# Kernel optimization log

Hardware: AMD Instinct MI355X
Metric: run time of the kernel (lower is better)

Reference implementation:

```python
import jax, jax.numpy as jnp
import numpy as np

B, H, W, C_IN, F = 4, 64, 64, 128, 256


def setup_inputs() -> dict:
    key = jax.random.key(0)
    ks = jax.random.split(key, 6)
    return {
        "inputs": jax.random.normal(ks[0], (B, H, W, C_IN), dtype=jnp.float32),
        "W_proj": jax.random.normal(ks[1], (C_IN, F), dtype=jnp.float32) * 0.02,
        "b_proj": jnp.zeros((F,), dtype=jnp.float32),
        "W_q": jax.random.normal(ks[2], (F, F), dtype=jnp.float32) * 0.02,
        "b_q": jnp.zeros((F,), dtype=jnp.float32),
        "W_k": jax.random.normal(ks[3], (F, F), dtype=jnp.float32) * 0.02,
        "b_k": jnp.zeros((F,), dtype=jnp.float32),
        "W_v": jax.random.normal(ks[4], (F, F), dtype=jnp.float32) * 0.02,
        "b_v": jnp.zeros((F,), dtype=jnp.float32),
        "gamma": jax.random.uniform(ks[5], (1,), dtype=jnp.float32),
    }


def reference(inputs, W_proj, b_proj, W_q, b_q, W_k, b_k, W_v, b_v, gamma):
    # 1x1 conv projection (C_in -> filters) since input channels != filters
    x = jnp.einsum("bhwc,cf->bhwf", inputs, W_proj) + b_proj  # [B,H,W,F]
    q = jnp.einsum("bhwf,fg->bhwg", x, W_q) + b_q
    k = jnp.einsum("bhwf,fg->bhwg", x, W_k) + b_k
    v = jnp.einsum("bhwf,fg->bhwg", x, W_v) + b_v
    b, h, w, f = x.shape
    n = h * w
    qr = q.reshape(b, n, f)
    kr = k.reshape(b, n, f)
    vr = v.reshape(b, n, f)
    attn = jax.nn.softmax(jnp.einsum("bnf,bmf->bnm", qr, kr), axis=-1)  # [B,N,N]
    context = jnp.einsum("bnm,bmf->bnf", attn, vr).reshape(b, h, w, f)
    return gamma * context + x
```

## Files before the change

kernel.cpp:

```cpp
#include <hip/hip_runtime.h>
#include <hip/hip_bf16.h>
#include <stdint.h>

typedef __attribute__((ext_vector_type(8))) short short8;
typedef __attribute__((ext_vector_type(4))) float floatx4;
typedef __attribute__((ext_vector_type(16))) float floatx16;
typedef __attribute__((ext_vector_type(2))) long longx2;

#define DEVI __device__ __forceinline__
#define MFMA16(a, b, c) __builtin_amdgcn_mfma_f32_16x16x32_bf16((a), (b), (c), 0, 0, 0)
#define MFMA32(a, b, c) __builtin_amdgcn_mfma_f32_32x32x16_fp8_fp8((a), (b), (c), 0, 0, 0)

typedef __attribute__((address_space(3))) unsigned int lds_u32;
typedef __attribute__((address_space(1))) const unsigned int glb_u32;
#define GLOAD_LDS16(g, l) __builtin_amdgcn_global_load_lds((glb_u32*)(g), (lds_u32*)(l), 16, 0, 0)

DEVI unsigned short f2bf(float x) {
    union { float f; unsigned int u; } v; v.f = x;
    unsigned int r = v.u + 0x7FFFu + ((v.u >> 16) & 1u);
    return (unsigned short)(r >> 16);
}
DEVI float bf2f(unsigned short h) {
    union { unsigned int u; float f; } v; v.u = ((unsigned int)h) << 16;
    return v.f;
}
DEVI unsigned char f2fp8(float x) {
    int c = __builtin_amdgcn_cvt_pk_fp8_f32(x, x, 0, false);
    return (unsigned char)(c & 0xFF);
}

__global__ __launch_bounds__(256) void prep_weights(
    const float* __restrict__ Wp, const float* __restrict__ Wq,
    const float* __restrict__ Wk, const float* __restrict__ Wv,
    unsigned short* __restrict__ Tp, unsigned short* __restrict__ Tq,
    unsigned short* __restrict__ Tk, unsigned short* __restrict__ Tv)
{
    __shared__ unsigned short Tl[64][72];
    const int bb = blockIdx.x;
    const float* W; unsigned short* T; int K; int tt;
    if (bb < 8)       { W = Wp; T = Tp; K = 128; tt = bb;      }
    else if (bb < 24) { W = Wq; T = Tq; K = 256; tt = bb - 8;  }
    else if (bb < 40) { W = Wk; T = Tk; K = 256; tt = bb - 24; }
    else              { W = Wv; T = Tv; K = 256; tt = bb - 40; }
    const int r0 = (tt >> 2) * 64;
    const int c0 = (tt & 3) * 64;
    const int tid = threadIdx.x;

    #pragma unroll
    for (int i = 0; i < 4; ++i) {
        int u = tid + i * 256;
        int r = u >> 4, c4 = u & 15;
        float4 v = *(const float4*)&W[(size_t)(r0 + r) * 256 + c0 + c4 * 4];
        Tl[c4 * 4 + 0][r] = f2bf(v.x);
        Tl[c4 * 4 + 1][r] = f2bf(v.y);
        Tl[c4 * 4 + 2][r] = f2bf(v.z);
        Tl[c4 * 4 + 3][r] = f2bf(v.w);
    }
    __syncthreads();
    #pragma unroll
    for (int i = 0; i < 2; ++i) {
        int u = tid + i * 256;
        int orow = u >> 3, g = u & 7;
        *(short8*)&T[(size_t)(c0 + orow) * K + r0 + g * 8] = *(const short8*)&Tl[orow][g * 8];
    }
}


__global__ __launch_bounds__(256) void gemm_bias(
    const float* __restrict__ A,
    const unsigned short* __restrict__ Wt,
    const float* __restrict__ bias,
    unsigned short* __restrict__ Cb,
    int N)
{
    __shared__ __align__(16) unsigned short As[64][136];
    __shared__ __align__(16) unsigned short Bs[64][136];
    const int tid  = threadIdx.x;
    const int w    = tid >> 6;
    const int lane = tid & 63;
    const int quad = lane >> 4;
    const int l15  = lane & 15;
    const int m0 = blockIdx.x * 64;
    const int n0 = blockIdx.y * 64;

    floatx4 acc[4];
    #pragma unroll
    for (int t = 0; t < 4; ++t) acc[t] = (floatx4)0.0f;

    #pragma unroll
    for (int it = 0; it < 8; ++it) {
        int idx = tid + it * 256;
        int r = idx >> 5, c4 = idx & 31;
        float4 v = *(const float4*)&A[(size_t)(m0 + r) * 128 + c4 * 4];
        ushort4 o;
        o.x = f2bf(v.x); o.y = f2bf(v.y); o.z = f2bf(v.z); o.w = f2bf(v.w);
        *(ushort4*)&As[r][c4 * 4] = o;
    }
    #pragma unroll
    for (int it = 0; it < 4; ++it) {
        int idx = tid + it * 256;
        int r = idx >> 4, g = idx & 15;
        *(short8*)&Bs[r][g * 8] = *(const short8*)&Wt[(size_t)(n0 + r) * 128 + g * 8];
    }
    __syncthreads();
    #pragma unroll
    for (int s = 0; s < 4; ++s) {
        short8 a = *(const short8*)&As[w * 16 + l15][s * 32 + quad * 8];
        #pragma unroll
        for (int t = 0; t < 4; ++t) {
            short8 bfr = *(const short8*)&Bs[t * 16 + l15][s * 32 + quad * 8];
            acc[t] = MFMA16(a, bfr, acc[t]);
        }
    }

    __syncthreads();
    unsigned short* T = &As[0][0];
    #pragma unroll
    for (int t = 0; t < 4; ++t) {
        int n = n0 + t * 16 + l15;
        float bs = bias[n];
        #pragma unroll
        for (int r = 0; r < 4; ++r)
            T[(w * 16 + quad * 4 + r) * 80 + t * 16 + l15] = f2bf(acc[t][r] + bs);
    }
    __syncthreads();
    int row = tid >> 2, c8 = (tid & 3) * 8;
    #pragma unroll
    for (int half = 0; half < 2; ++half) {
        int4 ov = *(const int4*)&T[row * 80 + c8 + half * 32];
        *(int4*)&Cb[(size_t)(m0 + row) * N + n0 + c8 + half * 32] = ov;
    }
}


__global__ __launch_bounds__(256) void gemm_qkv(
    const unsigned short* __restrict__ A,
    const unsigned short* __restrict__ Wt0, const unsigned short* __restrict__ Wt1, const unsigned short* __restrict__ Wt2,
    const float* __restrict__ b0, const float* __restrict__ b1, const float* __restrict__ b2,
    unsigned char* __restrict__ C0, unsigned char* __restrict__ C1, unsigned char* __restrict__ C2,
    int N)
{
    const unsigned short* Wt = (blockIdx.z == 0) ? Wt0 : (blockIdx.z == 1) ? Wt1 : Wt2;
    const float* bias        = (blockIdx.z == 0) ? b0  : (blockIdx.z == 1) ? b1  : b2;
    unsigned char* Cb        = (blockIdx.z == 0) ? C0  : (blockIdx.z == 1) ? C1  : C2;

    __shared__ __align__(16) unsigned short As[64][264];
    __shared__ __align__(16) unsigned short Bs[64][264];
    __shared__ __align__(16) unsigned char  Tt[64 * 80];
    const int tid  = threadIdx.x;
    const int w    = tid >> 6;
    const int lane = tid & 63;
    const int quad = lane >> 4;
    const int l15  = lane & 15;
    const int m0 = blockIdx.x * 64;

    #pragma unroll
    for (int it = 0; it < 8; ++it) {
        int u = tid + it * 256;
        int r = u >> 5, g = u & 31;
        *(short8*)&As[r][g * 8] = *(const short8*)&A[(size_t)(m0 + r) * 256 + g * 8];
    }

    const int b  = m0 >> 12;
    const int mt = (m0 & 4095) >> 5;

    for (int nt = 0; nt < 4; ++nt) {
        __syncthreads();
        #pragma unroll
        for (int it = 0; it < 8; ++it) {
            int u = tid + it * 256;
            int r = u >> 5, g = u & 31;
            *(short8*)&Bs[r][g * 8] = *(const short8*)&Wt[(size_t)(nt * 64 + r) * 256 + g * 8];
        }
        __syncthreads();

        floatx4 acc[4];
        #pragma unroll
        for (int t = 0; t < 4; ++t) acc[t] = (floatx4)0.0f;
        #pragma unroll
        for (int s = 0; s < 8; ++s) {
            short8 a = *(const short8*)&As[w * 16 + l15][s * 32 + quad * 8];
            #pragma unroll
            for (int t = 0; t < 4; ++t) {
                short8 bfr = *(const short8*)&Bs[t * 16 + l15][s * 32 + quad * 8];
                acc[t] = MFMA16(a, bfr, acc[t]);
            }
        }

        const int n0 = nt * 64;
        #pragma unroll
        for (int t = 0; t < 4; ++t) {
            int n = n0 + t * 16 + l15;
            float bs = bias[n];
            #pragma unroll
            for (int r = 0; r < 4; ++r)
                Tt[(w * 16 + quad * 4 + r) * 80 + t * 16 + l15] = f2fp8(acc[t][r] + bs);
        }
        __syncthreads();

        if (blockIdx.z == 0) {
            int row = tid >> 2, c16 = (tid & 3) * 16;
            int4 vq = *(const int4*)&Tt[row * 80 + c16];
            *(int4*)&Cb[(size_t)(m0 + row) * 256 + n0 + c16] = vq;
        } else {
            const int kt  = tid >> 7;
            const int sub = (tid >> 6) & 1;
            const int ln  = tid & 63;
            const int l31b = ln & 31, hib = ln >> 5;
            union { long h[2]; int4 v; unsigned char bts[16]; } o;
            if (blockIdx.z == 1) {
                #pragma unroll
                for (int h = 0; h < 2; ++h)
                    o.h[h] = *(const long*)&Tt[(kt * 32 + l31b) * 80 + (sub * 2 + h) * 16 + hib * 8];
            } else {
                #pragma unroll
                for (int s2 = 0; s2 < 2; ++s2)
                    #pragma unroll
                    for (int j = 0; j < 8; ++j)
                        o.bts[s2 * 8 + j] = Tt[(kt * 32 + s2 * 16 + hib * 8 + j) * 80 + sub * 32 + l31b];
            }
            unsigned char* dst = Cb + (size_t)b * 1048576 + (size_t)(mt + kt) * 8192
                               + (size_t)((n0 >> 5) + sub) * 1024 + ln * 16;
            *(int4*)dst = o.v;
        }
    }
}


__global__ __launch_bounds__(512, 2) void flash_attn(
    const unsigned char* __restrict__ qg,
    const unsigned char* __restrict__ kp,
    const unsigned char* __restrict__ vp,
    const unsigned short* __restrict__ xb,
    const float* __restrict__ gamma,
    float* __restrict__ out)
{
    __shared__ __align__(16) unsigned char KV[2][65536];
    float* MbF = (float*)&KV[0][0];
    float* Ml  = MbF + 64 * 264;

    const int tid  = threadIdx.x;
    const int w    = tid >> 6;
    const int lane = tid & 63;
    const int l31  = lane & 31;
    const int hi   = lane >> 5;
    const int kq   = w & 3;
    const int rw   = w >> 2;
    const int blk  = blockIdx.x;
    const int b    = (blk & 7) >> 1;
    const int rt   = (blk >> 3) * 2 + (blk & 1);
    const int row0 = rt * 64 + rw * 32;

    const size_t baseQ = ((size_t)b * 4096 + row0 + l31) * 256 + hi * 8;
    long qf[16];
    #pragma unroll
    for (int s = 0; s < 16; ++s)
        qf[s] = *(const long*)&qg[baseQ + s * 16];

    const long ones8 = 0x3838383838383838L;

    floatx16 ctx[8];
    #pragma unroll
    for (int i = 0; i < 8; ++i) ctx[i] = (floatx16)0.0f;
    floatx16 lacc = (floatx16)0.0f;

    const unsigned char* kb_b = kp + (size_t)b * 1048576;
    const unsigned char* vb_b = vp + (size_t)b * 1048576;

#define FA_STAGE(T, BUF)                                                             \
    {                                                                                \
        _Pragma("unroll")                                                            \
        for (int p = 0; p < 8; ++p) {                                                \
            const int c    = p * 8 + w;                                              \
            const int ckq  = c >> 4;                                                 \
            const int csel = (c >> 3) & 1;                                           \
            const int coff = (c & 7) * 1024;                                         \
            const unsigned char* src = (csel ? vb_b : kb_b)                          \
                + (size_t)ckq * 262144 + (size_t)(T) * 8192 + coff + lane * 16;      \
            GLOAD_LDS16(src, &KV[BUF][ckq * 16384 + csel * 8192 + coff]);            \
        }                                                                            \
    }

    FA_STAGE(0, 0)

    for (int t = 0; t < 32; ++t) {
        const int buf = t & 1;
        __syncthreads();
        if (t < 31) FA_STAGE(t + 1, buf ^ 1)

        const unsigned char* kc = &KV[buf][kq * 16384];
        const unsigned char* vc = &KV[buf][kq * 16384 + 8192];

        longx2 kk[8];
        #pragma unroll
        for (int p = 0; p < 8; ++p)
            kk[p] = *(const longx2*)&kc[p * 1024 + lane * 16];
        floatx16 sa = (floatx16)0.0f, sb = (floatx16)0.0f;
        __builtin_amdgcn_s_setprio(1);
        #pragma unroll
        for (int p = 0; p < 8; ++p) {
            sa = MFMA32(kk[p].x, qf[2 * p],     sa);
            sb = MFMA32(kk[p].y, qf[2 * p + 1], sb);
        }
        __builtin_amdgcn_s_setprio(0);

        float e[16];
        #pragma unroll
        for (int r = 0; r < 16; ++r) e[r] = __expf(sa[r] + sb[r]);
        int X0 = __builtin_amdgcn_cvt_pk_fp8_f32(e[0],  e[1],  0,  false);
        X0     = __builtin_amdgcn_cvt_pk_fp8_f32(e[2],  e[3],  X0, true);
        int Y0 = __builtin_amdgcn_cvt_pk_fp8_f32(e[4],  e[5],  0,  false);
        Y0     = __builtin_amdgcn_cvt_pk_fp8_f32(e[6],  e[7],  Y0, true);
        int X1 = __builtin_amdgcn_cvt_pk_fp8_f32(e[8],  e[9],  0,  false);
        X1     = __builtin_amdgcn_cvt_pk_fp8_f32(e[10], e[11], X1, true);
        int Y1 = __builtin_amdgcn_cvt_pk_fp8_f32(e[12], e[13], 0,  false);
        Y1     = __builtin_amdgcn_cvt_pk_fp8_f32(e[14], e[15], Y1, true);
        asm volatile("v_permlane32_swap_b32 %0, %1" : "+v"(X0), "+v"(Y0));
        asm volatile("v_permlane32_swap_b32 %0, %1" : "+v"(X1), "+v"(Y1));
        union { int i2[2]; long l; } u0, u1;
        u0.i2[0] = X0; u0.i2[1] = Y0;
        u1.i2[0] = X1; u1.i2[1] = Y1;
        const long ap0 = u0.l;
        const long ap1 = u1.l;

        lacc = MFMA32(ap0, ones8, lacc);
        lacc = MFMA32(ap1, ones8, lacc);
        __builtin_amdgcn_s_setprio(1);
        #pragma unroll
        for (int p = 0; p < 8; ++p) {
            longx2 vv = *(const longx2*)&vc[p * 1024 + lane * 16];
            ctx[p] = MFMA32(ap0, vv.x, ctx[p]);
            ctx[p] = MFMA32(ap1, vv.y, ctx[p]);
        }
        __builtin_amdgcn_s_setprio(0);
    }
#undef FA_STAGE

    __syncthreads();
    for (int pass = 3; pass >= 0; --pass) {
        if (kq == pass) {
            #pragma unroll
            for (int fb = 0; fb < 8; ++fb) {
                #pragma unroll
                for (int r = 0; r < 16; ++r) {
                    int row = rw * 32 + (r & 3) + 8 * (r >> 2) + 4 * hi;
                    int idx = row * 264 + fb * 32 + l31;
                    float prev = (pass == 3) ? 0.0f : MbF[idx];
                    MbF[idx] = prev + ctx[fb][r];
                }
            }
            if (l31 == 0) {
                #pragma unroll
                for (int r = 0; r < 16; ++r) {
                    int row = rw * 32 + (r & 3) + 8 * (r >> 2) + 4 * hi;
                    float prev = (pass == 3) ? 0.0f : Ml[row];
                    Ml[row] = prev + lacc[r];
                }
            }
        }
        __syncthreads();
    }

    const float g = gamma[0];
    const int row = tid >> 3;
    const int c0  = (tid & 7) * 32;
    const float rl = 1.0f / Ml[row];
    const size_t o = ((size_t)b * 4096 + rt * 64 + row) * 256 + c0;
    #pragma unroll
    for (int j = 0; j < 4; ++j) {
        short8 xv = *(const short8*)&xb[o + j * 8];
        float res[8];
        #pragma unroll
        for (int i = 0; i < 8; ++i)
            res[i] = g * MbF[row * 264 + c0 + j * 8 + i] * rl + bf2f((unsigned short)xv[i]);
        *(float4*)&out[o + j * 8]     = *(float4*)&res[0];
        *(float4*)&out[o + j * 8 + 4] = *(float4*)&res[4];
    }
}


extern "C" void kernel_launch(void* const* d_in, const int* in_sizes, int n_in,
                              void* d_out, int out_size, void* d_ws, size_t ws_size,
                              hipStream_t stream)
{
    const float* inp   = (const float*)d_in[0];
    const float* Wp    = (const float*)d_in[1];
    const float* bp    = (const float*)d_in[2];
    const float* Wq    = (const float*)d_in[3];
    const float* bq    = (const float*)d_in[4];
    const float* Wk    = (const float*)d_in[5];
    const float* bk    = (const float*)d_in[6];
    const float* Wv    = (const float*)d_in[7];
    const float* bv    = (const float*)d_in[8];
    const float* gamma = (const float*)d_in[9];
    float* out = (float*)d_out;

    char* ws = (char*)d_ws;
    unsigned char*  q8    = (unsigned char*)(ws + 0);
    unsigned char*  k8    = (unsigned char*)(ws + 4194304);
    unsigned char*  v8    = (unsigned char*)(ws + 8388608);
    unsigned short* x_b   = (unsigned short*)(ws + 12582912);
    unsigned short* Wt_p  = (unsigned short*)(ws + 20971520);
    unsigned short* Wt_q  = (unsigned short*)(ws + 21037056);
    unsigned short* Wt_k  = (unsigned short*)(ws + 21168128);
    unsigned short* Wt_v  = (unsigned short*)(ws + 21299200);

    prep_weights<<<56, 256, 0, stream>>>(Wp, Wq, Wk, Wv, Wt_p, Wt_q, Wt_k, Wt_v);
    gemm_bias<<<dim3(256, 4), 256, 0, stream>>>(inp, Wt_p, bp, x_b, 256);
    gemm_qkv<<<dim3(256, 1, 3), 256, 0, stream>>>(x_b, Wt_q, Wt_k, Wt_v, bq, bk, bv,
                                                  q8, k8, v8, 256);
    flash_attn<<<256, 512, 0, stream>>>(q8, k8, v8, x_b, gamma, out);
}
```

Before: 187.8 us.

## Fuse all four stages into one cooperative persistent kernel with grid syncs

Merges the weight prep, projection GEMM, QKV GEMM and flash attention kernels into one cooperative kernel of 256 blocks of 512 threads, separated by grid-wide barriers. The goal is to remove the launch gaps and tail effects between the four launches. In exchange, the GEMM phases run in a 512-thread, 128KB-LDS configuration that limits occupancy, and the QKV GEMM now splits K into chunks, adding extra barriers. Each grid.sync also has a fixed cost.

```diff
diff --git a/kernel.cpp b/kernel.cpp
--- a/kernel.cpp
+++ b/kernel.cpp
@@ -1,6 +1,9 @@
 #include <hip/hip_runtime.h>
 #include <hip/hip_bf16.h>
+#include <hip/hip_cooperative_groups.h>
 #include <stdint.h>
+
+namespace cg = cooperative_groups;
 
 typedef __attribute__((ext_vector_type(8))) short short8;
 typedef __attribute__((ext_vector_type(4))) float floatx4;
@@ -29,352 +32,337 @@
     return (unsigned char)(c & 0xFF);
 }
 
-__global__ __launch_bounds__(256) void prep_weights(
-    const float* __restrict__ Wp, const float* __restrict__ Wq,
-    const float* __restrict__ Wk, const float* __restrict__ Wv,
-    unsigned short* __restrict__ Tp, unsigned short* __restrict__ Tq,
-    unsigned short* __restrict__ Tk, unsigned short* __restrict__ Tv)
-{
-    __shared__ unsigned short Tl[64][72];
-    const int bb = blockIdx.x;
-    const float* W; unsigned short* T; int K; int tt;
-    if (bb < 8)       { W = Wp; T = Tp; K = 128; tt = bb;      }
-    else if (bb < 24) { W = Wq; T = Tq; K = 256; tt = bb - 8;  }
-    else if (bb < 40) { W = Wk; T = Tk; K = 256; tt = bb - 24; }
-    else              { W = Wv; T = Tv; K = 256; tt = bb - 40; }
-    const int r0 = (tt >> 2) * 64;
-    const int c0 = (tt & 3) * 64;
-    const int tid = threadIdx.x;
-
-    #pragma unroll
-    for (int i = 0; i < 4; ++i) {
-        int u = tid + i * 256;
-        int r = u >> 4, c4 = u & 15;
-        float4 v = *(const float4*)&W[(size_t)(r0 + r) * 256 + c0 + c4 * 4];
-        Tl[c4 * 4 + 0][r] = f2bf(v.x);
-        Tl[c4 * 4 + 1][r] = f2bf(v.y);
-        Tl[c4 * 4 + 2][r] = f2bf(v.z);
-        Tl[c4 * 4 + 3][r] = f2bf(v.w);
-    }
-    __syncthreads();
-    #pragma unroll
-    for (int i = 0; i < 2; ++i) {
-        int u = tid + i * 256;
-        int orow = u >> 3, g = u & 7;
-        *(short8*)&T[(size_t)(c0 + orow) * K + r0 + g * 8] = *(const short8*)&Tl[orow][g * 8];
-    }
-}
-
-
-__global__ __launch_bounds__(256) void gemm_bias(
-    const float* __restrict__ A,
-    const unsigned short* __restrict__ Wt,
-    const float* __restrict__ bias,
-    unsigned short* __restrict__ Cb,
-    int N)
-{
-    __shared__ __align__(16) unsigned short As[64][136];
-    __shared__ __align__(16) unsigned short Bs[64][136];
-    const int tid  = threadIdx.x;
-    const int w    = tid >> 6;
-    const int lane = tid & 63;
-    const int quad = lane >> 4;
-    const int l15  = lane & 15;
-    const int m0 = blockIdx.x * 64;
-    const int n0 = blockIdx.y * 64;
-
-    floatx4 acc[4];
-    #pragma unroll
-    for (int t = 0; t < 4; ++t) acc[t] = (floatx4)0.0f;
-
-    #pragma unroll
-    for (int it = 0; it < 8; ++it) {
-        int idx = tid + it * 256;
-        int r = idx >> 5, c4 = idx & 31;
-        float4 v = *(const float4*)&A[(size_t)(m0 + r) * 128 + c4 * 4];
-        ushort4 o;
-        o.x = f2bf(v.x); o.y = f2bf(v.y); o.z = f2bf(v.z); o.w = f2bf(v.w);
-        *(ushort4*)&As[r][c4 * 4] = o;
-    }
-    #pragma unroll
-    for (int it = 0; it < 4; ++it) {
-        int idx = tid + it * 256;
-        int r = idx >> 4, g = idx & 15;
-        *(short8*)&Bs[r][g * 8] = *(const short8*)&Wt[(size_t)(n0 + r) * 128 + g * 8];
-    }
-    __syncthreads();
-    #pragma unroll
-    for (int s = 0; s < 4; ++s) {
-        short8 a = *(const short8*)&As[w * 16 + l15][s * 32 + quad * 8];
-        #pragma unroll
-        for (int t = 0; t < 4; ++t) {
-            short8 bfr = *(const short8*)&Bs[t * 16 + l15][s * 32 + quad * 8];
-            acc[t] = MFMA16(a, bfr, acc[t]);
-        }
-    }
-
-    __syncthreads();
-    unsigned short* T = &As[0][0];
-    #pragma unroll
-    for (int t = 0; t < 4; ++t) {
-        int n = n0 + t * 16 + l15;
-        float bs = bias[n];
-        #pragma unroll
-        for (int r = 0; r < 4; ++r)
-            T[(w * 16 + quad * 4 + r) * 80 + t * 16 + l15] = f2bf(acc[t][r] + bs);
-    }
-    __syncthreads();
-    int row = tid >> 2, c8 = (tid & 3) * 8;
-    #pragma unroll
-    for (int half = 0; half < 2; ++half) {
-        int4 ov = *(const int4*)&T[row * 80 + c8 + half * 32];
-        *(int4*)&Cb[(size_t)(m0 + row) * N + n0 + c8 + half * 32] = ov;
-    }
-}
-
-
-__global__ __launch_bounds__(256) void gemm_qkv(
-    const unsigned short* __restrict__ A,
-    const unsigned short* __restrict__ Wt0, const unsigned short* __restrict__ Wt1, const unsigned short* __restrict__ Wt2,
-    const float* __restrict__ b0, const float* __restrict__ b1, const float* __restrict__ b2,
-    unsigned char* __restrict__ C0, unsigned char* __restrict__ C1, unsigned char* __restrict__ C2,
-    int N)
-{
-    const unsigned short* Wt = (blockIdx.z == 0) ? Wt0 : (blockIdx.z == 1) ? Wt1 : Wt2;
-    const float* bias        = (blockIdx.z == 0) ? b0  : (blockIdx.z == 1) ? b1  : b2;
-    unsigned char* Cb        = (blockIdx.z == 0) ? C0  : (blockIdx.z == 1) ? C1  : C2;
-
-    __shared__ __align__(16) unsigned short As[64][264];
-    __shared__ __align__(16) unsigned short Bs[64][264];
-    __shared__ __align__(16) unsigned char  Tt[64 * 80];
-    const int tid  = threadIdx.x;
-    const int w    = tid >> 6;
-    const int lane = tid & 63;
-    const int quad = lane >> 4;
-    const int l15  = lane & 15;
-    const int m0 = blockIdx.x * 64;
-
-    #pragma unroll
-    for (int it = 0; it < 8; ++it) {
-        int u = tid + it * 256;
-        int r = u >> 5, g = u & 31;
-        *(short8*)&As[r][g * 8] = *(const short8*)&A[(size_t)(m0 + r) * 256 + g * 8];
-    }
-
-    const int b  = m0 >> 12;
-    const int mt = (m0 & 4095) >> 5;
-
-    for (int nt = 0; nt < 4; ++nt) {
-        __syncthreads();
-        #pragma unroll
-        for (int it = 0; it < 8; ++it) {
-            int u = tid + it * 256;
-            int r = u >> 5, g = u & 31;
-            *(short8*)&Bs[r][g * 8] = *(const short8*)&Wt[(size_t)(nt * 64 + r) * 256 + g * 8];
-        }
-        __syncthreads();
-
-        floatx4 acc[4];
-        #pragma unroll
-        for (int t = 0; t < 4; ++t) acc[t] = (floatx4)0.0f;
-        #pragma unroll
-        for (int s = 0; s < 8; ++s) {
-            short8 a = *(const short8*)&As[w * 16 + l15][s * 32 + quad * 8];
-            #pragma unroll
-            for (int t = 0; t < 4; ++t) {
-                short8 bfr = *(const short8*)&Bs[t * 16 + l15][s * 32 + quad * 8];
-                acc[t] = MFMA16(a, bfr, acc[t]);
-            }
-        }
-
-        const int n0 = nt * 64;
-        #pragma unroll
-        for (int t = 0; t < 4; ++t) {
-            int n = n0 + t * 16 + l15;
-            float bs = bias[n];
-            #pragma unroll
-            for (int r = 0; r < 4; ++r)
-                Tt[(w * 16 + quad * 4 + r) * 80 + t * 16 + l15] = f2fp8(acc[t][r] + bs);
-        }
-        __syncthreads();
-
-        if (blockIdx.z == 0) {
-            int row = tid >> 2, c16 = (tid & 3) * 16;
-            int4 vq = *(const int4*)&Tt[row * 80 + c16];
-            *(int4*)&Cb[(size_t)(m0 + row) * 256 + n0 + c16] = vq;
-        } else {
-            const int kt  = tid >> 7;
-            const int sub = (tid >> 6) & 1;
-            const int ln  = tid & 63;
-            const int l31b = ln & 31, hib = ln >> 5;
-            union { long h[2]; int4 v; unsigned char bts[16]; } o;
-            if (blockIdx.z == 1) {
-                #pragma unroll
-                for (int h = 0; h < 2; ++h)
-                    o.h[h] = *(const long*)&Tt[(kt * 32 + l31b) * 80 + (sub * 2 + h) * 16 + hib * 8];
-            } else {
-                #pragma unroll
-                for (int s2 = 0; s2 < 2; ++s2)
-                    #pragma unroll
-                    for (int j = 0; j < 8; ++j)
-                        o.bts[s2 * 8 + j] = Tt[(kt * 32 + s2 * 16 + hib * 8 + j) * 80 + sub * 32 + l31b];
-            }
-            unsigned char* dst = Cb + (size_t)b * 1048576 + (size_t)(mt + kt) * 8192
-                               + (size_t)((n0 >> 5) + sub) * 1024 + ln * 16;
-            *(int4*)dst = o.v;
-        }
-    }
-}
-
-
-__global__ __launch_bounds__(512, 2) void flash_attn(
-    const unsigned char* __restrict__ qg,
-    const unsigned char* __restrict__ kp,
-    const unsigned char* __restrict__ vp,
-    const unsigned short* __restrict__ xb,
+
+__global__ __launch_bounds__(512, 2) void fused_all(
+    const float* __restrict__ inp,
+    const float* __restrict__ Wp, const float* __restrict__ bp,
+    const float* __restrict__ Wq, const float* __restrict__ bq,
+    const float* __restrict__ Wk, const float* __restrict__ bk,
+    const float* __restrict__ Wv, const float* __restrict__ bv,
     const float* __restrict__ gamma,
+    unsigned short* __restrict__ Wt_p, unsigned short* __restrict__ Wt_q,
+    unsigned short* __restrict__ Wt_k, unsigned short* __restrict__ Wt_v,
+    unsigned short* __restrict__ xb,
+    unsigned char* __restrict__ q8, unsigned char* __restrict__ k8,
+    unsigned char* __restrict__ v8,
     float* __restrict__ out)
 {
-    __shared__ __align__(16) unsigned char KV[2][65536];
-    float* MbF = (float*)&KV[0][0];
-    float* Ml  = MbF + 64 * 264;
-
-    const int tid  = threadIdx.x;
-    const int w    = tid >> 6;
-    const int lane = tid & 63;
-    const int l31  = lane & 31;
-    const int hi   = lane >> 5;
-    const int kq   = w & 3;
-    const int rw   = w >> 2;
-    const int blk  = blockIdx.x;
-    const int b    = (blk & 7) >> 1;
-    const int rt   = (blk >> 3) * 2 + (blk & 1);
-    const int row0 = rt * 64 + rw * 32;
-
-    const size_t baseQ = ((size_t)b * 4096 + row0 + l31) * 256 + hi * 8;
-    long qf[16];
-    #pragma unroll
-    for (int s = 0; s < 16; ++s)
-        qf[s] = *(const long*)&qg[baseQ + s * 16];
-
-    const long ones8 = 0x3838383838383838L;
-
-    floatx16 ctx[8];
-    #pragma unroll
-    for (int i = 0; i < 8; ++i) ctx[i] = (floatx16)0.0f;
-    floatx16 lacc = (floatx16)0.0f;
-
-    const unsigned char* kb_b = kp + (size_t)b * 1048576;
-    const unsigned char* vb_b = vp + (size_t)b * 1048576;
+    __shared__ __align__(16) unsigned char SMEM[131072];
+    cg::grid_group grid = cg::this_grid();
+
+    const int tid = threadIdx.x;
+    const int blk = blockIdx.x;
+
+    if (blk < 56) {
+        const float* W; unsigned short* T; int K; int tt;
+        if (blk < 8)       { W = Wp; T = Wt_p; K = 128; tt = blk;      }
+        else if (blk < 24) { W = Wq; T = Wt_q; K = 256; tt = blk - 8;  }
+        else if (blk < 40) { W = Wk; T = Wt_k; K = 256; tt = blk - 24; }
+        else               { W = Wv; T = Wt_v; K = 256; tt = blk - 40; }
+        const int r0 = (tt >> 2) * 64, c0 = (tt & 3) * 64;
+        unsigned short (*Tl)[72] = (unsigned short (*)[72])SMEM;
+        #pragma unroll
+        for (int i = 0; i < 2; ++i) {
+            int u = tid + i * 512;
+            int r = u >> 4, c4 = u & 15;
+            float4 v = *(const float4*)&W[(size_t)(r0 + r) * 256 + c0 + c4 * 4];
+            Tl[c4 * 4 + 0][r] = f2bf(v.x);
+            Tl[c4 * 4 + 1][r] = f2bf(v.y);
+            Tl[c4 * 4 + 2][r] = f2bf(v.z);
+            Tl[c4 * 4 + 3][r] = f2bf(v.w);
+        }
+        __syncthreads();
+        {
+            int orow = tid >> 3, g = tid & 7;
+            *(short8*)&T[(size_t)(c0 + orow) * K + r0 + g * 8] = *(const short8*)&Tl[orow][g * 8];
+        }
+    }
+    __threadfence();
+    grid.sync();
+
+    {
+        const int half = tid >> 8;
+        const int t    = tid & 255;
+        const int w    = t >> 6;
+        const int lane = t & 63;
+        const int quad = lane >> 4;
+        const int l15  = lane & 15;
+        const int m0   = blk * 64;
+        unsigned short* As = (unsigned short*)(SMEM + half * 40960);
+        unsigned short* Bs = As + 64 * 136;
+
+        #pragma unroll
+        for (int itn = 0; itn < 2; ++itn) {
+            const int n0 = (itn * 2 + half) * 64;
+            floatx4 acc[4];
+            #pragma unroll
+            for (int q = 0; q < 4; ++q) acc[q] = (floatx4)0.0f;
+
+            #pragma unroll
+            for (int i = 0; i < 8; ++i) {
+                int idx = t + i * 256;
+                int r = idx >> 5, c4 = idx & 31;
+                float4 v = *(const float4*)&inp[(size_t)(m0 + r) * 128 + c4 * 4];
+                ushort4 o;
+                o.x = f2bf(v.x); o.y = f2bf(v.y); o.z = f2bf(v.z); o.w = f2bf(v.w);
+                *(ushort4*)&As[r * 136 + c4 * 4] = o;
+            }
+            #pragma unroll
+            for (int i = 0; i < 4; ++i) {
+                int idx = t + i * 256;
+                int r = idx >> 4, g = idx & 15;
+                *(short8*)&Bs[r * 136 + g * 8] = *(const short8*)&Wt_p[(size_t)(n0 + r) * 128 + g * 8];
+            }
+            __syncthreads();
+            #pragma unroll
+            for (int s = 0; s < 4; ++s) {
+                short8 a = *(const short8*)&As[(w * 16 + l15) * 136 + s * 32 + quad * 8];
+                #pragma unroll
+                for (int q = 0; q < 4; ++q) {
+                    short8 bfr = *(const short8*)&Bs[(q * 16 + l15) * 136 + s * 32 + quad * 8];
+                    acc[q] = MFMA16(a, bfr, acc[q]);
+                }
+            }
+            __syncthreads();
+            unsigned short* T = As;
+            #pragma unroll
+            for (int q = 0; q < 4; ++q) {
+                int n = n0 + q * 16 + l15;
+                float bs = bp[n];
+                #pragma unroll
+                for (int r = 0; r < 4; ++r)
+                    T[(w * 16 + quad * 4 + r) * 80 + q * 16 + l15] = f2bf(acc[q][r] + bs);
+            }
+            __syncthreads();
+            {
+                int row = t >> 2, c8 = (t & 3) * 8;
+                #pragma unroll
+                for (int hh = 0; hh < 2; ++hh) {
+                    int4 ov = *(const int4*)&T[row * 80 + c8 + hh * 32];
+                    *(int4*)&xb[(size_t)(m0 + row) * 256 + n0 + c8 + hh * 32] = ov;
+                }
+            }
+            __syncthreads();
+        }
+
+        const int b  = m0 >> 12;
+        const int mt = (m0 & 4095) >> 5;
+        for (int itk = 0; itk < 6; ++itk) {
+            const int task = itk * 2 + half;
+            const int op = task >> 2, n0 = (task & 3) * 64;
+            const unsigned short* Wt = (op == 0) ? Wt_q : (op == 1) ? Wt_k : Wt_v;
+            const float* bias        = (op == 0) ? bq   : (op == 1) ? bk   : bv;
+            unsigned char* Cb        = (op == 0) ? q8   : (op == 1) ? k8   : v8;
+
+            floatx4 acc[4];
+            #pragma unroll
+            for (int q = 0; q < 4; ++q) acc[q] = (floatx4)0.0f;
+
+            for (int kc = 0; kc < 256; kc += 128) {
+                __syncthreads();
+                #pragma unroll
+                for (int i = 0; i < 4; ++i) {
+                    int idx = t + i * 256;
+                    int r = idx >> 4, g = idx & 15;
+                    *(short8*)&As[r * 136 + g * 8] = *(const short8*)&xb[(size_t)(m0 + r) * 256 + kc + g * 8];
+                    *(short8*)&Bs[r * 136 + g * 8] = *(const short8*)&Wt[(size_t)(n0 + r) * 256 + kc + g * 8];
+                }
+                __syncthreads();
+                #pragma unroll
+                for (int s = 0; s < 4; ++s) {
+                    short8 a = *(const short8*)&As[(w * 16 + l15) * 136 + s * 32 + quad * 8];
+                    #pragma unroll
+                    for (int q = 0; q < 4; ++q) {
+                        short8 bfr = *(const short8*)&Bs[(q * 16 + l15) * 136 + s * 32 + quad * 8];
+                        acc[q] = MFMA16(a, bfr, acc[q]);
+                    }
+                }
+            }
+
+            __syncthreads();
+            unsigned char* T = (unsigned char*)As;
+            #pragma unroll
+            for (int q = 0; q < 4; ++q) {
+                int n = n0 + q * 16 + l15;
+                float bs = bias[n];
+                #pragma unroll
+                for (int r = 0; r < 4; ++r)
+                    T[(w * 16 + quad * 4 + r) * 80 + q * 16 + l15] = f2fp8(acc[q][r] + bs);
+            }
+            __syncthreads();
+
+            if (op == 0) {
+                int row = t >> 2, c16 = (t & 3) * 16;
+                int4 vq = *(const int4*)&T[row * 80 + c16];
+                *(int4*)&Cb[(size_t)(m0 + row) * 256 + n0 + c16] = vq;
+            } else {
+                const int kt  = t >> 7;
+                const int sub = (t >> 6) & 1;
+                const int ln  = t & 63;
+                const int l31b = ln & 31, hib = ln >> 5;
+                union { long h[2]; int4 v; unsigned char bts[16]; } o;
+                if (op == 1) {
+                    #pragma unroll
+                    for (int hh = 0; hh < 2; ++hh)
+                        o.h[hh] = *(const long*)&T[(kt * 32 + l31b) * 80 + (sub * 2 + hh) * 16 + hib * 8];
+                } else {
+                    #pragma unroll
+                    for (int s2 = 0; s2 < 2; ++s2)
+                        #pragma unroll
+                        for (int j = 0; j < 8; ++j)
+                            o.bts[s2 * 8 + j] = T[(kt * 32 + s2 * 16 + hib * 8 + j) * 80 + sub * 32 + l31b];
+                }
+                unsigned char* dst = Cb + (size_t)b * 1048576 + (size_t)(mt + kt) * 8192
+                                   + (size_t)((n0 >> 5) + sub) * 1024 + ln * 16;
+                *(int4*)dst = o.v;
+            }
+            __syncthreads();
+        }
+    }
+
+    __threadfence();
+    grid.sync();
+
+    {
+        unsigned char (*KV)[65536] = (unsigned char (*)[65536])SMEM;
+        float* MbF = (float*)SMEM;
+        float* Ml  = MbF + 64 * 264;
+
+        const int fw   = tid >> 6;
+        const int ln   = tid & 63;
+        const int l31  = ln & 31;
+        const int hi   = ln >> 5;
+        const int kq   = fw & 3;
+        const int rw   = fw >> 2;
+        const int b    = (blk & 7) >> 1;
+        const int rt   = (blk >> 3) * 2 + (blk & 1);
+        const int row0 = rt * 64 + rw * 32;
+
+        const size_t baseQ = ((size_t)b * 4096 + row0 + l31) * 256 + hi * 8;
+        long qf[16];
+        #pragma unroll
+        for (int s = 0; s < 16; ++s)
+            qf[s] = *(const long*)&q8[baseQ + s * 16];
+
+        const long ones8 = 0x3838383838383838L;
+
+        floatx16 ctx[8];
+        #pragma unroll
+        for (int i = 0; i < 8; ++i) ctx[i] = (floatx16)0.0f;
+        floatx16 lacc = (floatx16)0.0f;
+
+        const unsigned char* kb_b = k8 + (size_t)b * 1048576;
+        const unsigned char* vb_b = v8 + (size_t)b * 1048576;
 
 #define FA_STAGE(T, BUF)                                                             \
     {                                                                                \
         _Pragma("unroll")                                                            \
         for (int p = 0; p < 8; ++p) {                                                \
-            const int c    = p * 8 + w;                                              \
+            const int c    = p * 8 + fw;                                             \
             const int ckq  = c >> 4;                                                 \
             const int csel = (c >> 3) & 1;                                           \
             const int coff = (c & 7) * 1024;                                         \
             const unsigned char* src = (csel ? vb_b : kb_b)                          \
-                + (size_t)ckq * 262144 + (size_t)(T) * 8192 + coff + lane * 16;      \
+                + (size_t)ckq * 262144 + (size_t)(T) * 8192 + coff + ln * 16;        \
             GLOAD_LDS16(src, &KV[BUF][ckq * 16384 + csel * 8192 + coff]);            \
         }                                                                            \
     }
 
-    FA_STAGE(0, 0)
-
-    for (int t = 0; t < 32; ++t) {
-        const int buf = t & 1;
+        FA_STAGE(0, 0)
+
+        for (int ti = 0; ti < 32; ++ti) {
+            const int buf = ti & 1;
+            __syncthreads();
+            if (ti < 31) FA_STAGE(ti + 1, buf ^ 1)
+
+            const unsigned char* kc = &KV[buf][kq * 16384];
+            const unsigned char* vc = &KV[buf][kq * 16384 + 8192];
+
+            longx2 kk[8];
+            #pragma unroll
+            for (int p = 0; p < 8; ++p)
+                kk[p] = *(const longx2*)&kc[p * 1024 + ln * 16];
+            floatx16 sa = (floatx16)0.0f, sb = (floatx16)0.0f;
+            __builtin_amdgcn_s_setprio(1);
+            #pragma unroll
+            for (int p = 0; p < 8; ++p) {
+                sa = MFMA32(kk[p].x, qf[2 * p],     sa);
+                sb = MFMA32(kk[p].y, qf[2 * p + 1], sb);
+            }
+            __builtin_amdgcn_s_setprio(0);
+
+            float e[16];
+            #pragma unroll
+            for (int r = 0; r < 16; ++r) e[r] = __expf(sa[r] + sb[r]);
+            int X0 = __builtin_amdgcn_cvt_pk_fp8_f32(e[0],  e[1],  0,  false);
+            X0     = __builtin_amdgcn_cvt_pk_fp8_f32(e[2],  e[3],  X0, true);
+            int Y0 = __builtin_amdgcn_cvt_pk_fp8_f32(e[4],  e[5],  0,  false);
+            Y0     = __builtin_amdgcn_cvt_pk_fp8_f32(e[6],  e[7],  Y0, true);
+            int X1 = __builtin_amdgcn_cvt_pk_fp8_f32(e[8],  e[9],  0,  false);
+            X1     = __builtin_amdgcn_cvt_pk_fp8_f32(e[10], e[11], X1, true);
+            int Y1 = __builtin_amdgcn_cvt_pk_fp8_f32(e[12], e[13], 0,  false);
+            Y1     = __builtin_amdgcn_cvt_pk_fp8_f32(e[14], e[15], Y1, true);
+            asm volatile("v_permlane32_swap_b32 %0, %1" : "+v"(X0), "+v"(Y0));
+            asm volatile("v_permlane32_swap_b32 %0, %1" : "+v"(X1), "+v"(Y1));
+            union { int i2[2]; long l; } u0, u1;
+            u0.i2[0] = X0; u0.i2[1] = Y0;
+            u1.i2[0] = X1; u1.i2[1] = Y1;
+            const long ap0 = u0.l;
+            const long ap1 = u1.l;
+
+            lacc = MFMA32(ap0, ones8, lacc);
+            lacc = MFMA32(ap1, ones8, lacc);
+            __builtin_amdgcn_s_setprio(1);
+            #pragma unroll
+            for (int p = 0; p < 8; ++p) {
+                longx2 vv = *(const longx2*)&vc[p * 1024 + ln * 16];
+                ctx[p] = MFMA32(ap0, vv.x, ctx[p]);
+                ctx[p] = MFMA32(ap1, vv.y, ctx[p]);
+            }
+            __builtin_amdgcn_s_setprio(0);
+        }
+#undef FA_STAGE
+
         __syncthreads();
-        if (t < 31) FA_STAGE(t + 1, buf ^ 1)
-
-        const unsigned char* kc = &KV[buf][kq * 16384];
-        const unsigned char* vc = &KV[buf][kq * 16384 + 8192];
-
-        longx2 kk[8];
+        for (int pass = 3; pass >= 0; --pass) {
+            if (kq == pass) {
+                #pragma unroll
+                for (int fb = 0; fb < 8; ++fb) {
+                    #pragma unroll
+                    for (int r = 0; r < 16; ++r) {
+                        int row = rw * 32 + (r & 3) + 8 * (r >> 2) + 4 * hi;
+                        int idx = row * 264 + fb * 32 + l31;
+                        float prev = (pass == 3) ? 0.0f : MbF[idx];
+                        MbF[idx] = prev + ctx[fb][r];
+                    }
+                }
+                if (l31 == 0) {
+                    #pragma unroll
+                    for (int r = 0; r < 16; ++r) {
+                        int row = rw * 32 + (r & 3) + 8 * (r >> 2) + 4 * hi;
+                        float prev = (pass == 3) ? 0.0f : Ml[row];
+                        Ml[row] = prev + lacc[r];
+                    }
+                }
+            }
+            __syncthreads();
+        }
+
+        const float g = gamma[0];
+        const int row = tid >> 3;
+        const int c0  = (tid & 7) * 32;
+        const float rl = 1.0f / Ml[row];
+        const size_t o = ((size_t)b * 4096 + rt * 64 + row) * 256 + c0;
         #pragma unroll
-        for (int p = 0; p < 8; ++p)
-            kk[p] = *(const longx2*)&kc[p * 1024 + lane * 16];
-        floatx16 sa = (floatx16)0.0f, sb = (floatx16)0.0f;
-        __builtin_amdgcn_s_setprio(1);
-        #pragma unroll
-        for (int p = 0; p < 8; ++p) {
-            sa = MFMA32(kk[p].x, qf[2 * p],     sa);
-            sb = MFMA32(kk[p].y, qf[2 * p + 1], sb);
-        }
-        __builtin_amdgcn_s_setprio(0);
-
-        float e[16];
-        #pragma unroll
-        for (int r = 0; r < 16; ++r) e[r] = __expf(sa[r] + sb[r]);
-        int X0 = __builtin_amdgcn_cvt_pk_fp8_f32(e[0],  e[1],  0,  false);
-        X0     = __builtin_amdgcn_cvt_pk_fp8_f32(e[2],  e[3],  X0, true);
-        int Y0 = __builtin_amdgcn_cvt_pk_fp8_f32(e[4],  e[5],  0,  false);
-        Y0     = __builtin_amdgcn_cvt_pk_fp8_f32(e[6],  e[7],  Y0, true);
-        int X1 = __builtin_amdgcn_cvt_pk_fp8_f32(e[8],  e[9],  0,  false);
-        X1     = __builtin_amdgcn_cvt_pk_fp8_f32(e[10], e[11], X1, true);
-        int Y1 = __builtin_amdgcn_cvt_pk_fp8_f32(e[12], e[13], 0,  false);
-        Y1     = __builtin_amdgcn_cvt_pk_fp8_f32(e[14], e[15], Y1, true);
-        asm volatile("v_permlane32_swap_b32 %0, %1" : "+v"(X0), "+v"(Y0));
-        asm volatile("v_permlane32_swap_b32 %0, %1" : "+v"(X1), "+v"(Y1));
-        union { int i2[2]; long l; } u0, u1;
-        u0.i2[0] = X0; u0.i2[1] = Y0;
-        u1.i2[0] = X1; u1.i2[1] = Y1;
-        const long ap0 = u0.l;
-        const long ap1 = u1.l;
-
-        lacc = MFMA32(ap0, ones8, lacc);
-        lacc = MFMA32(ap1, ones8, lacc);
-        __builtin_amdgcn_s_setprio(1);
-        #pragma unroll
-        for (int p = 0; p < 8; ++p) {
-            longx2 vv = *(const longx2*)&vc[p * 1024 + lane * 16];
-            ctx[p] = MFMA32(ap0, vv.x, ctx[p]);
-            ctx[p] = MFMA32(ap1, vv.y, ctx[p]);
-        }
-        __builtin_amdgcn_s_setprio(0);
-    }
-#undef FA_STAGE
-
-    __syncthreads();
-    for (int pass = 3; pass >= 0; --pass) {
-        if (kq == pass) {
-            #pragma unroll
-            for (int fb = 0; fb < 8; ++fb) {
-                #pragma unroll
-                for (int r = 0; r < 16; ++r) {
-                    int row = rw * 32 + (r & 3) + 8 * (r >> 2) + 4 * hi;
-                    int idx = row * 264 + fb * 32 + l31;
-                    float prev = (pass == 3) ? 0.0f : MbF[idx];
-                    MbF[idx] = prev + ctx[fb][r];
-                }
-            }
-            if (l31 == 0) {
-                #pragma unroll
-                for (int r = 0; r < 16; ++r) {
-                    int row = rw * 32 + (r & 3) + 8 * (r >> 2) + 4 * hi;
-                    float prev = (pass == 3) ? 0.0f : Ml[row];
-                    Ml[row] = prev + lacc[r];
-                }
-            }
-        }
-        __syncthreads();
-    }
-
-    const float g = gamma[0];
-    const int row = tid >> 3;
-    const int c0  = (tid & 7) * 32;
-    const float rl = 1.0f / Ml[row];
-    const size_t o = ((size_t)b * 4096 + rt * 64 + row) * 256 + c0;
-    #pragma unroll
-    for (int j = 0; j < 4; ++j) {
-        short8 xv = *(const short8*)&xb[o + j * 8];
-        float res[8];
-        #pragma unroll
-        for (int i = 0; i < 8; ++i)
-            res[i] = g * MbF[row * 264 + c0 + j * 8 + i] * rl + bf2f((unsigned short)xv[i]);
-        *(float4*)&out[o + j * 8]     = *(float4*)&res[0];
-        *(float4*)&out[o + j * 8 + 4] = *(float4*)&res[4];
+        for (int j = 0; j < 4; ++j) {
+            short8 xv = *(const short8*)&xb[o + j * 8];
+            float res[8];
+            #pragma unroll
+            for (int i = 0; i < 8; ++i)
+                res[i] = g * MbF[row * 264 + c0 + j * 8 + i] * rl + bf2f((unsigned short)xv[i]);
+            *(float4*)&out[o + j * 8]     = *(float4*)&res[0];
+            *(float4*)&out[o + j * 8 + 4] = *(float4*)&res[4];
+        }
     }
 }
 
@@ -405,9 +393,12 @@
     unsigned short* Wt_k  = (unsigned short*)(ws + 21168128);
     unsigned short* Wt_v  = (unsigned short*)(ws + 21299200);
 
-    prep_weights<<<56, 256, 0, stream>>>(Wp, Wq, Wk, Wv, Wt_p, Wt_q, Wt_k, Wt_v);
-    gemm_bias<<<dim3(256, 4), 256, 0, stream>>>(inp, Wt_p, bp, x_b, 256);
-    gemm_qkv<<<dim3(256, 1, 3), 256, 0, stream>>>(x_b, Wt_q, Wt_k, Wt_v, bq, bk, bv,
-                                                  q8, k8, v8, 256);
-    flash_attn<<<256, 512, 0, stream>>>(q8, k8, v8, x_b, gamma, out);
+    void* args[] = {
+        (void*)&inp, (void*)&Wp, (void*)&bp, (void*)&Wq, (void*)&bq,
+        (void*)&Wk, (void*)&bk, (void*)&Wv, (void*)&bv, (void*)&gamma,
+        (void*)&Wt_p, (void*)&Wt_q, (void*)&Wt_k, (void*)&Wt_v,
+        (void*)&x_b, (void*)&q8, (void*)&k8, (void*)&v8, (void*)&out
+    };
+    hipLaunchCooperativeKernel((const void*)fused_all, dim3(256), dim3(512),
+                               args, 0, stream);
 }
```

Result: slower. 358.3 us (+90.8%).
